# Optimization experiments

Measured on AMD Instinct MI355X. Metric: run time of the kernel, lower is better.

The kernel has to match this reference:

```python
import jax, jax.numpy as jnp
import numpy as np
from jax import lax

S = 8192      # total tokens
HID = 1280    # hidden_size
H = 16        # num_heads
D = HID // H  # head_dim = 80
NSEG = 8      # number of equal-length segments (images)


def rotate_half(x):
    half = x.shape[-1] // 2
    return jnp.concatenate([-x[..., half:], x[..., :half]], axis=-1)


def setup_inputs() -> dict:
    key = jax.random.key(0)
    k1, k2, k3, k4 = jax.random.split(key, 4)
    hidden_states = jax.random.normal(k1, (S, HID), dtype=jnp.float32)
    # rotary embeddings: angles repeated over both halves, as in standard vision RoPE
    theta = jax.random.uniform(k2, (S, D // 2), dtype=jnp.float32) * (2.0 * np.pi)
    freqs = jnp.concatenate([theta, theta], axis=-1)  # [S, D]
    cos = jnp.cos(freqs)
    sin = jnp.sin(freqs)
    qkv_kernel = jax.random.normal(k3, (HID, 3, H, D), dtype=jnp.float32) * 0.02
    qkv_bias = jnp.zeros((3, H, D), dtype=jnp.float32)
    proj_kernel = jax.random.normal(k4, (H * D, HID), dtype=jnp.float32) * 0.02
    proj_bias = jnp.zeros((HID,), dtype=jnp.float32)
    cu_seqlens = jnp.arange(NSEG + 1, dtype=jnp.int32) * (S // NSEG)
    return {
        "hidden_states": hidden_states, "cos": cos, "sin": sin,
        "qkv_kernel": qkv_kernel, "qkv_bias": qkv_bias,
        "proj_kernel": proj_kernel, "proj_bias": proj_bias,
        "cu_seqlens": cu_seqlens,
    }


def reference(hidden_states, cos, sin, qkv_kernel, qkv_bias, proj_kernel, proj_bias, cu_seqlens):
    P = lax.Precision.HIGHEST
    seq, dtype = hidden_states.shape[0], hidden_states.dtype
    # fused QKV projection: [S, 3, H, D]
    qkv = jnp.einsum('sd,dtnh->stnh', hidden_states, qkv_kernel, precision=P) + qkv_bias
    q, k, v = qkv[:, 0], qkv[:, 1], qkv[:, 2]
    # rotary position embedding in fp32 (as in original)
    cf = cos[:, None, :].astype(jnp.float32)
    sf = sin[:, None, :].astype(jnp.float32)
    qf = q.astype(jnp.float32)
    kf = k.astype(jnp.float32)
    q = (qf * cf + rotate_half(qf) * sf).astype(dtype)
    k = (kf * cf + rotate_half(kf) * sf).astype(dtype)
    # block-diagonal attention over equal-length segments from cu_seqlens
    n_seg = cu_seqlens.shape[0] - 1
    L = seq // n_seg  # segment length (uniform segments)
    head_dim = q.shape[-1]
    scale = head_dim ** (-0.5)
    qs = q.reshape(n_seg, L, H, head_dim)
    ks = k.reshape(n_seg, L, H, head_dim)
    vs = v.reshape(n_seg, L, H, head_dim)
    logits = jnp.einsum('bqhd,bkhd->bhqk', qs, ks, precision=P) * scale
    attn = jax.nn.softmax(logits.astype(jnp.float32), axis=-1).astype(dtype)
    out = jnp.einsum('bhqk,bkhd->bqhd', attn, vs, precision=P).reshape(seq, H * head_dim)
    return jnp.einsum('se,ed->sd', out, proj_kernel, precision=P) + proj_bias
```

## Files before the change

kernel.cpp:

```cpp
#include <hip/hip_runtime.h>

#define S_LEN 8192
#define HID   1280
#define NHEAD 16
#define HD    80
#define NQKV  3840
#define VTS   8256

#define GLOBAL_AS __attribute__((address_space(1)))
#define LDS_AS    __attribute__((address_space(3)))

typedef __attribute__((ext_vector_type(8))) short bf16x8;
typedef __attribute__((ext_vector_type(4))) float f32x4;
typedef __attribute__((ext_vector_type(4))) unsigned short u16x4;
typedef __attribute__((ext_vector_type(8))) unsigned short u16x8;
typedef __attribute__((ext_vector_type(2))) unsigned int u32x2;

__device__ __forceinline__ unsigned short f2bf(float f) {
    union { float f; unsigned int u; } v; v.f = f;
    unsigned int r = v.u + 0x7FFFu + ((v.u >> 16) & 1u);
    return (unsigned short)(r >> 16);
}
__device__ __forceinline__ float bf2f(unsigned short h) {
    union { unsigned int u; float f; } v; v.u = ((unsigned int)h) << 16;
    return v.f;
}
__device__ __forceinline__ unsigned int cvt_pk_bf16(float a, float b) {
    unsigned int r;
    asm("v_cvt_pk_bf16_f32 %0, %1, %2" : "=v"(r) : "v"(a), "v"(b));
    return r;
}

__global__ __launch_bounds__(256) void k_cvt(const float* __restrict__ src,
                                             unsigned short* __restrict__ dst,
                                             unsigned short* __restrict__ vbz, int n4)
{
    int i = blockIdx.x * 256 + threadIdx.x;
    if (blockIdx.x == 0 && threadIdx.x < 4)
        ((u16x8*)vbz)[threadIdx.x] = (u16x8)(unsigned short)0;
    if (i >= n4) return;
    f32x4 v = *(const f32x4*)&src[(size_t)i * 4];
    u16x4 o;
    o[0] = f2bf(v[0]); o[1] = f2bf(v[1]); o[2] = f2bf(v[2]); o[3] = f2bf(v[3]);
    *(u16x4*)&dst[(size_t)i * 4] = o;
}

__global__ __launch_bounds__(256) void k_wt(const float* __restrict__ W,
                                            unsigned short* __restrict__ Wt,
                                            int R, int C)
{
    __shared__ float T[32][33];
    int r0 = blockIdx.y * 32, c0 = blockIdx.x * 32;
    int tr = threadIdx.x >> 3, tc = (threadIdx.x & 7) * 4;
    f32x4 v = *(const f32x4*)&W[(size_t)(r0 + tr) * C + c0 + tc];
    T[tr][tc + 0] = v[0]; T[tr][tc + 1] = v[1];
    T[tr][tc + 2] = v[2]; T[tr][tc + 3] = v[3];
    __syncthreads();
    int c = threadIdx.x >> 3, r4 = (threadIdx.x & 7) * 4;
    u16x4 o;
    o[0] = f2bf(T[r4 + 0][c]); o[1] = f2bf(T[r4 + 1][c]);
    o[2] = f2bf(T[r4 + 2][c]); o[3] = f2bf(T[r4 + 3][c]);
    *(u16x4*)&Wt[(size_t)(c0 + c) * R + r0 + r4] = o;
}

__global__ __launch_bounds__(512, 2) void k_qkv256(
    const unsigned short* __restrict__ A,
    const unsigned short* __restrict__ Bt,
    const float* __restrict__ bias,
    unsigned short* __restrict__ q0, unsigned short* __restrict__ k0p,
    unsigned short* __restrict__ vt)
{
    __shared__ __align__(16) unsigned short As[2][2][16][64][8];
    __shared__ __align__(16) unsigned short Bs[2][2][16][64][8];
    const int tid = threadIdx.x;
    const int w = tid >> 6, l = tid & 63;
    const int qg = l & 15, g = l >> 4;
    const int wm = w >> 2, wn = w & 3;
    const int wm8 = wm * 8, wn4 = wn * 4;

    const int bid = blockIdx.x;
    const int xcd = bid & 7, t = bid >> 3;
    const int bm0 = (xcd * 4 + (t & 3)) * 256;
    const int bn0 = (t >> 2) * 256;

    const unsigned short* ga = A + (size_t)(bm0 + w * 16 + qg) * HID + g * 8;
    const unsigned short* gb = Bt + (size_t)(bn0 + w * 16 + qg) * HID + g * 8;

#define SG_A(d, ks, kcol) do {                                                  \
    __builtin_amdgcn_global_load_lds((const GLOBAL_AS unsigned int*)(ga + (kcol)), \
        (LDS_AS unsigned int*)&As[d][ks][w][0][0], 16, 0, 0);                   \
    __builtin_amdgcn_global_load_lds((const GLOBAL_AS unsigned int*)(ga + (size_t)128 * HID + (kcol)), \
        (LDS_AS unsigned int*)&As[d][ks][8 + w][0][0], 16, 0, 0); } while (0)
#define SG_B(d, ks, kcol) do {                                                  \
    __builtin_amdgcn_global_load_lds((const GLOBAL_AS unsigned int*)(gb + (kcol)), \
        (LDS_AS unsigned int*)&Bs[d][ks][w][0][0], 16, 0, 0);                   \
    __builtin_amdgcn_global_load_lds((const GLOBAL_AS unsigned int*)(gb + (size_t)128 * HID + (kcol)), \
        (LDS_AS unsigned int*)&Bs[d][ks][8 + w][0][0], 16, 0, 0); } while (0)

#define RD_A4(d, ks, fb) do {                                                   \
    af[0] = *(const bf16x8*)&As[d][ks][wm8 + (fb) + 0][l][0];                   \
    af[1] = *(const bf16x8*)&As[d][ks][wm8 + (fb) + 1][l][0];                   \
    af[2] = *(const bf16x8*)&As[d][ks][wm8 + (fb) + 2][l][0];                   \
    af[3] = *(const bf16x8*)&As[d][ks][wm8 + (fb) + 3][l][0]; } while (0)
#define RD_B4(d, ks) do {                                                       \
    bf[0] = *(const bf16x8*)&Bs[d][ks][wn4 + 0][l][0];                          \
    bf[1] = *(const bf16x8*)&Bs[d][ks][wn4 + 1][l][0];                          \
    bf[2] = *(const bf16x8*)&Bs[d][ks][wn4 + 2][l][0];                          \
    bf[3] = *(const bf16x8*)&Bs[d][ks][wn4 + 3][l][0]; } while (0)

#define MFMAQ(base) do {                                                        \
    _Pragma("unroll")                                                           \
    for (int m = 0; m < 4; ++m)                                                 \
        _Pragma("unroll")                                                       \
        for (int n = 0; n < 4; ++n)                                             \
            acc[(base) + m][n] = __builtin_amdgcn_mfma_f32_16x16x32_bf16(       \
                af[m], bf[n], acc[(base) + m][n], 0, 0, 0); } while (0)

#define BARW() do { __builtin_amdgcn_s_barrier();                               \
    asm volatile("s_waitcnt lgkmcnt(0)" ::: "memory");                          \
    __builtin_amdgcn_sched_barrier(0);                                          \
    __builtin_amdgcn_s_setprio(1); } while (0)
#define BARC() do { __builtin_amdgcn_s_setprio(0);                              \
    __builtin_amdgcn_s_barrier();                                               \
    __builtin_amdgcn_sched_barrier(0); } while (0)
#define BARC_VM4() do { __builtin_amdgcn_s_setprio(0);                          \
    asm volatile("s_waitcnt vmcnt(4)" ::: "memory");                            \
    __builtin_amdgcn_s_barrier();                                               \
    __builtin_amdgcn_sched_barrier(0); } while (0)
#define BARC_VM0() do { __builtin_amdgcn_s_setprio(0);                          \
    asm volatile("s_waitcnt vmcnt(0)" ::: "memory");                            \
    __builtin_amdgcn_s_barrier();                                               \
    __builtin_amdgcn_sched_barrier(0); } while (0)

    f32x4 acc[8][4];
#pragma unroll
    for (int m = 0; m < 8; ++m)
#pragma unroll
        for (int n = 0; n < 4; ++n) acc[m][n] = (f32x4){0.f, 0.f, 0.f, 0.f};

    SG_A(0, 0, 0);  SG_B(0, 0, 0);
    SG_A(0, 1, 32); SG_B(0, 1, 32);
    SG_A(1, 0, 64); SG_B(1, 0, 64);
    asm volatile("s_waitcnt vmcnt(4)" ::: "memory");
    __builtin_amdgcn_s_barrier();
    __builtin_amdgcn_sched_barrier(0);

    const int NIT = HID / 128;
    for (int j = 0; j < NIT; ++j) {
        const bool st = (j + 1 < NIT);
        const int c1 = j * 128 + 96;
        const int c2 = j * 128 + 128;
        const int c2b = j * 128 + 160;
        const int c3 = j * 128 + 192;
        bf16x8 af[4], bf[4];

        RD_A4(0, 0, 0); RD_B4(0, 0);
        SG_A(1, 1, c1);
        BARW(); MFMAQ(0); BARC();
        RD_A4(0, 0, 4);
        SG_B(1, 1, c1);
        BARW(); MFMAQ(4); BARC();
        RD_A4(0, 1, 0); RD_B4(0, 1);
        if (st) SG_A(0, 0, c2);
        BARW(); MFMAQ(0); BARC();
        RD_A4(0, 1, 4);
        if (st) SG_B(0, 0, c2);
        BARW(); MFMAQ(4);
        if (st) BARC_VM4(); else BARC_VM0();
        RD_A4(1, 0, 0); RD_B4(1, 0);
        if (st) SG_A(0, 1, c2b);
        BARW(); MFMAQ(0); BARC();
        RD_A4(1, 0, 4);
        if (st) SG_B(0, 1, c2b);
        BARW(); MFMAQ(4); BARC();
        RD_A4(1, 1, 0); RD_B4(1, 1);
        if (st) SG_A(1, 0, c3);
        BARW(); MFMAQ(0); BARC();
        RD_A4(1, 1, 4);
        if (st) SG_B(1, 0, c3);
        BARW(); MFMAQ(4);
        if (st) BARC_VM4(); else BARC_VM0();
    }
#undef SG_A
#undef SG_B
#undef RD_A4
#undef RD_B4
#undef MFMAQ
#undef BARW
#undef BARC
#undef BARC_VM4
#undef BARC_VM0

    const int t3 = bn0 / HID;
    if (t3 < 2) {
        unsigned short* dst = (t3 == 0) ? q0 : k0p;
        const int colbase = bn0 - t3 * HID + wn * 64 + qg;
        float bv[4];
#pragma unroll
        for (int n = 0; n < 4; ++n) bv[n] = bias[bn0 + wn * 64 + n * 16 + qg];
#pragma unroll
        for (int m = 0; m < 8; ++m)
#pragma unroll
            for (int r = 0; r < 4; ++r) {
                const int row = bm0 + wm * 128 + m * 16 + g * 4 + r;
                unsigned short* drow = dst + (size_t)row * HID + colbase;
#pragma unroll
                for (int n = 0; n < 4; ++n)
                    drow[n * 16] = f2bf(acc[m][n][r] + bv[n]);
            }
    } else {
        const int colbase = bn0 - 2 * HID + wn * 64;
#pragma unroll
        for (int n = 0; n < 4; ++n) {
            const int vcol = colbase + n * 16 + qg;
            const float bv = bias[bn0 + wn * 64 + n * 16 + qg];
            unsigned short* dcol = vt + (size_t)vcol * VTS + bm0 + wm * 128 + g * 4;
#pragma unroll
            for (int m = 0; m < 8; ++m) {
                u16x4 o;
#pragma unroll
                for (int r = 0; r < 4; ++r) o[r] = f2bf(acc[m][n][r] + bv);
                *(u16x4*)&dcol[m * 16] = o;
            }
        }
    }
}

__global__ __launch_bounds__(256) void k_rope(
    unsigned short* __restrict__ qb, unsigned short* __restrict__ kb,
    const float* __restrict__ cosb, const float* __restrict__ sinb)
{
    const float SCQ = 0.11180339887498949f * 1.44269504088896340f;
    int idx = blockIdx.x * 256 + threadIdx.x;
    if (idx >= S_LEN * NHEAD * 10) return;
    int s = idx / 160;
    int rem = idx - s * 160;
    int nh = rem / 10, h4 = (rem - nh * 10) * 4;
    size_t base = (size_t)s * HID + nh * HD + h4;
    f32x4 c0 = *(const f32x4*)&cosb[s * HD + h4];
    f32x4 c1 = *(const f32x4*)&cosb[s * HD + h4 + 40];
    f32x4 s0 = *(const f32x4*)&sinb[s * HD + h4];
    f32x4 s1 = *(const f32x4*)&sinb[s * HD + h4 + 40];
    u16x4 qa = *(const u16x4*)&qb[base];
    u16x4 qb4 = *(const u16x4*)&qb[base + 40];
    u16x4 ka = *(const u16x4*)&kb[base];
    u16x4 kb4 = *(const u16x4*)&kb[base + 40];
    u16x4 o0, o1, p0, p1;
#pragma unroll
    for (int j = 0; j < 4; ++j) {
        float qaf = bf2f(qa[j]), qbf = bf2f(qb4[j]);
        o0[j] = f2bf((qaf * c0[j] - qbf * s0[j]) * SCQ);
        o1[j] = f2bf((qbf * c1[j] + qaf * s1[j]) * SCQ);
        float kaf = bf2f(ka[j]), kbf = bf2f(kb4[j]);
        p0[j] = f2bf(kaf * c0[j] - kbf * s0[j]);
        p1[j] = f2bf(kbf * c1[j] + kaf * s1[j]);
    }
    *(u16x4*)&qb[base] = o0;
    *(u16x4*)&qb[base + 40] = o1;
    *(u16x4*)&kb[base] = p0;
    *(u16x4*)&kb[base + 40] = p1;
}

__global__ __launch_bounds__(256) void k_attn(
    const unsigned short* __restrict__ qb, const unsigned short* __restrict__ kbuf,
    const unsigned short* __restrict__ vt, unsigned short* __restrict__ ao)
{
    __shared__ __align__(16) unsigned short Ks[2][64][104];
    __shared__ __align__(16) unsigned short Vs[2][80][64];
    __shared__ __align__(16) unsigned short Pls[4][2][16][68];

    const int tid = threadIdx.x;
    const int w = tid >> 6, l = tid & 63;
    const int qg = l & 15, g = l >> 4;
    const int wb = w << 6;
    const int vxor = (qg & 7) << 4;

    const int b = blockIdx.x;
    const int xcd = b & 7, j = b >> 3;
    const int p = xcd * 16 + (j >> 3);
    const int qt = j & 7;
    const int seg = p >> 4, head = p & 15;
    const int row0 = seg * 1024 + qt * 128 + w * 32;
    const size_t hoff = (size_t)head * HD;
    const int vhead = head * HD;
    const int kb0 = seg * 1024;

#define STAGE(bi, kr0_)                                                        \
    {                                                                          \
        const int kr0s = (kr0_);                                               \
        _Pragma("unroll")                                                      \
        for (int i = 0; i < 4; ++i) {                                          \
            const int u = i * 256 + tid;                                       \
            if (u < 832) {                                                     \
                const int r = u / 13, cu = (u - r * 13) * 8;                   \
                __builtin_amdgcn_global_load_lds(                              \
                    (const GLOBAL_AS unsigned int*)&kbuf[(size_t)(kr0s + r) * HID + hoff + cu], \
                    (LDS_AS unsigned int*)((LDS_AS unsigned short*)&Ks[bi][0][0] + (size_t)(i * 256 + wb) * 8), \
                    16, 0, 0);                                                 \
            }                                                                  \
        }                                                                      \
        _Pragma("unroll")                                                      \
        for (int i = 0; i < 3; ++i) {                                          \
            const int u = i * 256 + tid;                                       \
            if (u < 640) {                                                     \
                const int r = u >> 3;                                          \
                const int cs = ((u & 7) * 16) ^ ((r & 7) << 4);                \
                __builtin_amdgcn_global_load_lds(                              \
                    (const GLOBAL_AS unsigned int*)&vt[(size_t)(vhead + r) * VTS + kr0s + (cs >> 1)], \
                    (LDS_AS unsigned int*)((LDS_AS unsigned short*)&Vs[bi][0][0] + (size_t)(i * 256 + wb) * 8), \
                    16, 0, 0);                                                 \
            }                                                                  \
        }                                                                      \
    }

#define COMPUTE(bi)                                                            \
    {                                                                          \
        f32x4 st[2][4];                                                        \
        _Pragma("unroll")                                                      \
        for (int s = 0; s < 2; ++s)                                            \
            _Pragma("unroll")                                                  \
            for (int kn = 0; kn < 4; ++kn) st[s][kn] = (f32x4){0.f, 0.f, 0.f, 0.f}; \
        __builtin_amdgcn_s_setprio(1);                                         \
        _Pragma("unroll")                                                      \
        for (int ks = 0; ks < 3; ++ks)                                         \
            _Pragma("unroll")                                                  \
            for (int kn = 0; kn < 4; ++kn) {                                   \
                bf16x8 kf = *(const bf16x8*)&Ks[bi][kn * 16 + qg][ks * 32 + g * 8]; \
                st[0][kn] = __builtin_amdgcn_mfma_f32_16x16x32_bf16(kf, qf[0][ks], st[0][kn], 0, 0, 0); \
                st[1][kn] = __builtin_amdgcn_mfma_f32_16x16x32_bf16(kf, qf[1][ks], st[1][kn], 0, 0, 0); \
            }                                                                  \
        __builtin_amdgcn_s_setprio(0);                                         \
        _Pragma("unroll")                                                      \
        for (int s = 0; s < 2; ++s) {                                          \
            float psum = 0.f;                                                  \
            _Pragma("unroll")                                                  \
            for (int kn = 0; kn < 4; ++kn) {                                   \
                float p0 = exp2f(st[s][kn][0]);                                \
                float p1 = exp2f(st[s][kn][1]);                                \
                float p2 = exp2f(st[s][kn][2]);                                \
                float p3 = exp2f(st[s][kn][3]);                                \
                psum += (p0 + p1) + (p2 + p3);                                 \
                u32x2 pk;                                                      \
                pk[0] = cvt_pk_bf16(p0, p1);                                   \
                pk[1] = cvt_pk_bf16(p2, p3);                                   \
                *(u32x2*)&Pls[w][s][qg][kn * 16 + g * 4] = pk;                 \
            }                                                                  \
            psum += __shfl_xor(psum, 16, 64);                                  \
            psum += __shfl_xor(psum, 32, 64);                                  \
            lsum[s] += psum;                                                   \
        }                                                                      \
        __builtin_amdgcn_s_setprio(1);                                         \
        _Pragma("unroll")                                                      \
        for (int ks = 0; ks < 2; ++ks) {                                       \
            bf16x8 pf0 = *(const bf16x8*)&Pls[w][0][qg][ks * 32 + g * 8];      \
            bf16x8 pf1 = *(const bf16x8*)&Pls[w][1][qg][ks * 32 + g * 8];      \
            _Pragma("unroll")                                                  \
            for (int d = 0; d < 5; ++d) {                                      \
                bf16x8 vf = *(const bf16x8*)((const unsigned short*)&Vs[bi][0][0] + \
                    (d * 16 + qg) * 64 + (((ks * 64 + g * 16) ^ vxor) >> 1));  \
                acc[0][d] = __builtin_amdgcn_mfma_f32_16x16x32_bf16(vf, pf0, acc[0][d], 0, 0, 0); \
                acc[1][d] = __builtin_amdgcn_mfma_f32_16x16x32_bf16(vf, pf1, acc[1][d], 0, 0, 0); \
            }                                                                  \
        }                                                                      \
        __builtin_amdgcn_s_setprio(0);                                         \
    }

    bf16x8 qf[2][3];
#pragma unroll
    for (int s = 0; s < 2; ++s)
#pragma unroll
        for (int ks = 0; ks < 3; ++ks) {
            if (ks < 2 || g < 2)
                qf[s][ks] = *(const bf16x8*)&qb[(size_t)(row0 + s * 16 + qg) * HID + hoff + ks * 32 + g * 8];
            else
                qf[s][ks] = (bf16x8)(short)0;
        }

    float lsum[2] = {0.f, 0.f};
    f32x4 acc[2][5];
#pragma unroll
    for (int s = 0; s < 2; ++s)
#pragma unroll
        for (int d = 0; d < 5; ++d) acc[s][d] = (f32x4){0.f, 0.f, 0.f, 0.f};

    STAGE(0, kb0);
    __syncthreads();
    for (int ch = 0; ch < 16; ch += 2) {
        if (ch + 1 < 16) STAGE(1, kb0 + (ch + 1) * 64);
        COMPUTE(0);
        __syncthreads();
        if (ch + 2 < 16) STAGE(0, kb0 + (ch + 2) * 64);
        COMPUTE(1);
        __syncthreads();
    }

#pragma unroll
    for (int s = 0; s < 2; ++s) {
        const float inv = 1.0f / lsum[s];
        const int orow = row0 + s * 16 + qg;
#pragma unroll
        for (int d = 0; d < 5; ++d) {
            u16x4 o;
#pragma unroll
            for (int r = 0; r < 4; ++r) o[r] = f2bf(acc[s][d][r] * inv);
            *(u16x4*)&ao[(size_t)orow * HID + hoff + d * 16 + g * 4] = o;
        }
    }
#undef STAGE
#undef COMPUTE
}

__global__ __launch_bounds__(256) void k_proj(
    const unsigned short* __restrict__ A,
    const unsigned short* __restrict__ Bt,
    const float* __restrict__ bias, float* __restrict__ out)
{
    __shared__ __align__(16) unsigned short As[128][32];
    __shared__ __align__(16) unsigned short Bs[128][32];
    const int tid = threadIdx.x;
    const int w = tid >> 6, l = tid & 63;
    const int qg = l & 15, g = l >> 4;
    const int wr = w >> 1, wc = w & 1;
    const int bid = blockIdx.x;
    const int xcd = bid & 7, t = bid >> 3;
    const int bm0 = (xcd * 8 + (t & 7)) * 128;
    const int bn0 = (t >> 3) * 128;

    f32x4 acc[4][4];
#pragma unroll
    for (int m = 0; m < 4; ++m)
#pragma unroll
        for (int n = 0; n < 4; ++n) acc[m][n] = (f32x4){0.f, 0.f, 0.f, 0.f};

    const int lr = l >> 2, lc = (l & 3) * 8;
    const unsigned short* ga = A + (size_t)(bm0 + w * 16 + lr) * HID + lc;
    const unsigned short* gb = Bt + (size_t)(bn0 + w * 16 + lr) * HID + lc;
    LDS_AS unsigned int* la0 = (LDS_AS unsigned int*)&As[w * 16][0];
    LDS_AS unsigned int* la1 = (LDS_AS unsigned int*)&As[w * 16 + 64][0];
    LDS_AS unsigned int* lb0 = (LDS_AS unsigned int*)&Bs[w * 16][0];
    LDS_AS unsigned int* lb1 = (LDS_AS unsigned int*)&Bs[w * 16 + 64][0];

    for (int k0 = 0; k0 < HID; k0 += 32) {
        __syncthreads();
        __builtin_amdgcn_global_load_lds((const GLOBAL_AS unsigned int*)(ga + k0), la0, 16, 0, 0);
        __builtin_amdgcn_global_load_lds((const GLOBAL_AS unsigned int*)(ga + (size_t)64 * HID + k0), la1, 16, 0, 0);
        __builtin_amdgcn_global_load_lds((const GLOBAL_AS unsigned int*)(gb + k0), lb0, 16, 0, 0);
        __builtin_amdgcn_global_load_lds((const GLOBAL_AS unsigned int*)(gb + (size_t)64 * HID + k0), lb1, 16, 0, 0);
        __syncthreads();
        bf16x8 af[4], bff[4];
#pragma unroll
        for (int m = 0; m < 4; ++m) af[m] = *(const bf16x8*)&As[wr * 64 + m * 16 + qg][g * 8];
#pragma unroll
        for (int n = 0; n < 4; ++n) bff[n] = *(const bf16x8*)&Bs[wc * 64 + n * 16 + qg][g * 8];
#pragma unroll
        for (int m = 0; m < 4; ++m)
#pragma unroll
            for (int n = 0; n < 4; ++n)
                acc[m][n] = __builtin_amdgcn_mfma_f32_16x16x32_bf16(af[m], bff[n], acc[m][n], 0, 0, 0);
    }

#pragma unroll
    for (int n = 0; n < 4; ++n) {
        const int col = bn0 + wc * 64 + n * 16 + qg;
        const float bv = bias[col];
#pragma unroll
        for (int m = 0; m < 4; ++m)
#pragma unroll
            for (int r = 0; r < 4; ++r) {
                const int row = bm0 + wr * 64 + m * 16 + g * 4 + r;
                out[(size_t)row * HID + col] = acc[m][n][r] + bv;
            }
    }
}

extern "C" void kernel_launch(void* const* d_in, const int* in_sizes, int n_in,
                              void* d_out, int out_size, void* d_ws, size_t ws_size,
                              hipStream_t stream)
{
    (void)in_sizes; (void)n_in; (void)out_size; (void)ws_size;
    const float* hidden = (const float*)d_in[0];
    const float* cosb   = (const float*)d_in[1];
    const float* sinb   = (const float*)d_in[2];
    const float* qkv_w  = (const float*)d_in[3];
    const float* qkv_b  = (const float*)d_in[4];
    const float* proj_w = (const float*)d_in[5];
    const float* proj_b = (const float*)d_in[6];

    float* out = (float*)d_out;
    unsigned short* ws = (unsigned short*)d_ws;
    const size_t n = (size_t)S_LEN * HID;
    unsigned short* hb     = ws;
    unsigned short* wqkvt  = hb + n;
    unsigned short* wprojt = wqkvt + (size_t)NQKV * HID;
    unsigned short* qb     = wprojt + (size_t)HID * HID;
    unsigned short* kb     = qb + n;
    unsigned short* vb     = kb + n;
    unsigned short* vt     = vb + n;
    unsigned short* aob    = vt + (size_t)NHEAD * HD * VTS;

    k_cvt<<<(int)((n / 4 + 255) / 256), 256, 0, stream>>>(hidden, hb, vb, (int)(n / 4));
    dim3 gw1(NQKV / 32, HID / 32);
    k_wt<<<gw1, 256, 0, stream>>>(qkv_w, wqkvt, HID, NQKV);
    dim3 gw2(HID / 32, HID / 32);
    k_wt<<<gw2, 256, 0, stream>>>(proj_w, wprojt, HID, HID);

    k_qkv256<<<480, 512, 0, stream>>>(hb, wqkvt, qkv_b, qb, kb, vt);

    k_rope<<<(S_LEN * NHEAD * 10 + 255) / 256, 256, 0, stream>>>(qb, kb, cosb, sinb);

    k_attn<<<1024, 256, 0, stream>>>(qb, kb, vt, aob);

    k_proj<<<640, 256, 0, stream>>>(aob, wprojt, proj_b, out);
}
```

Baseline: 255.3 us.

## Transpose softmax probabilities in registers via cross-lane shuffles instead of LDS

Removes the per-wave LDS staging buffer for the bf16 probability tile. The C-layout of the QK^T MFMA output is now rearranged into the B-operand layout for the PV MFMA with selects and two rounds of __shfl_xor, so no LDS writes or reads are needed. Dropping that buffer also cuts shared memory per block, and launch bounds now request 3 blocks per CU to raise occupancy. The cost is extra VALU/DPP shuffle work and register pressure, and the occupancy hint may force spills.

Measured after the change: 257.3 us. About the same (+0.8%).

```diff
diff --git a/kernel.cpp b/kernel.cpp
--- a/kernel.cpp
+++ b/kernel.cpp
@@ -15,6 +15,7 @@
 typedef __attribute__((ext_vector_type(4))) unsigned short u16x4;
 typedef __attribute__((ext_vector_type(8))) unsigned short u16x8;
 typedef __attribute__((ext_vector_type(2))) unsigned int u32x2;
+typedef __attribute__((ext_vector_type(4))) unsigned int u32x4;
 
 __device__ __forceinline__ unsigned short f2bf(float f) {
     union { float f; unsigned int u; } v; v.f = f;
@@ -261,19 +262,21 @@
     *(u16x4*)&kb[base + 40] = p1;
 }
 
-__global__ __launch_bounds__(256) void k_attn(
+__global__ __launch_bounds__(256, 3) void k_attn(
     const unsigned short* __restrict__ qb, const unsigned short* __restrict__ kbuf,
     const unsigned short* __restrict__ vt, unsigned short* __restrict__ ao)
 {
     __shared__ __align__(16) unsigned short Ks[2][64][104];
     __shared__ __align__(16) unsigned short Vs[2][80][64];
-    __shared__ __align__(16) unsigned short Pls[4][2][16][68];
 
     const int tid = threadIdx.x;
     const int w = tid >> 6, l = tid & 63;
     const int qg = l & 15, g = l >> 4;
     const int wb = w << 6;
     const int vxor = (qg & 7) << 4;
+    const bool bb = (g & 2) != 0;
+    const bool cb = ((g ^ (g >> 1)) & 1) != 0;
+    const bool og = (g & 1) != 0;
 
     const int b = blockIdx.x;
     const int xcd = b & 7, j = b >> 3;
@@ -330,9 +333,11 @@
                 st[1][kn] = __builtin_amdgcn_mfma_f32_16x16x32_bf16(kf, qf[1][ks], st[1][kn], 0, 0, 0); \
             }                                                                  \
         __builtin_amdgcn_s_setprio(0);                                         \
+        bf16x8 pfr[2][2];                                                      \
         _Pragma("unroll")                                                      \
         for (int s = 0; s < 2; ++s) {                                          \
             float psum = 0.f;                                                  \
+            unsigned int E[4][2];                                              \
             _Pragma("unroll")                                                  \
             for (int kn = 0; kn < 4; ++kn) {                                   \
                 float p0 = exp2f(st[s][kn][0]);                                \
@@ -340,20 +345,49 @@
                 float p2 = exp2f(st[s][kn][2]);                                \
                 float p3 = exp2f(st[s][kn][3]);                                \
                 psum += (p0 + p1) + (p2 + p3);                                 \
-                u32x2 pk;                                                      \
-                pk[0] = cvt_pk_bf16(p0, p1);                                   \
-                pk[1] = cvt_pk_bf16(p2, p3);                                   \
-                *(u32x2*)&Pls[w][s][qg][kn * 16 + g * 4] = pk;                 \
+                E[kn][0] = cvt_pk_bf16(p0, p1);                                \
+                E[kn][1] = cvt_pk_bf16(p2, p3);                                \
             }                                                                  \
             psum += __shfl_xor(psum, 16, 64);                                  \
             psum += __shfl_xor(psum, 32, 64);                                  \
             lsum[s] += psum;                                                   \
+            const unsigned int oc0x = bb ? E[1][0] : E[0][0];                  \
+            const unsigned int oc0y = bb ? E[1][1] : E[0][1];                  \
+            const unsigned int oc1x = bb ? E[3][0] : E[2][0];                  \
+            const unsigned int oc1y = bb ? E[3][1] : E[2][1];                  \
+            const unsigned int sa0x = bb ? E[0][0] : E[1][0];                  \
+            const unsigned int sa0y = bb ? E[0][1] : E[1][1];                  \
+            const unsigned int sa1x = bb ? E[2][0] : E[3][0];                  \
+            const unsigned int sa1y = bb ? E[2][1] : E[3][1];                  \
+            const unsigned int rx0x = __shfl_xor(sa0x, 32, 64);                \
+            const unsigned int rx0y = __shfl_xor(sa0y, 32, 64);                \
+            const unsigned int rx1x = __shfl_xor(sa1x, 32, 64);                \
+            const unsigned int rx1y = __shfl_xor(sa1y, 32, 64);                \
+            const unsigned int kp0x = cb ? rx0x : oc0x;                        \
+            const unsigned int kp0y = cb ? rx0y : oc0y;                        \
+            const unsigned int kp1x = cb ? rx1x : oc1x;                        \
+            const unsigned int kp1y = cb ? rx1y : oc1y;                        \
+            const unsigned int sb0x = cb ? oc0x : rx0x;                        \
+            const unsigned int sb0y = cb ? oc0y : rx0y;                        \
+            const unsigned int sb1x = cb ? oc1x : rx1x;                        \
+            const unsigned int sb1y = cb ? oc1y : rx1y;                        \
+            const unsigned int rb0x = __shfl_xor(sb0x, 16, 64);                \
+            const unsigned int rb0y = __shfl_xor(sb0y, 16, 64);                \
+            const unsigned int rb1x = __shfl_xor(sb1x, 16, 64);                \
+            const unsigned int rb1y = __shfl_xor(sb1y, 16, 64);                \
+            u32x4 t0, t1;                                                      \
+            t0[0] = og ? rb0x : kp0x; t0[1] = og ? rb0y : kp0y;                \
+            t0[2] = og ? kp0x : rb0x; t0[3] = og ? kp0y : rb0y;                \
+            t1[0] = og ? rb1x : kp1x; t1[1] = og ? rb1y : kp1y;                \
+            t1[2] = og ? kp1x : rb1x; t1[3] = og ? kp1y : rb1y;                \
+            pfr[s][0] = __builtin_bit_cast(bf16x8, t0);                        \
+            pfr[s][1] = __builtin_bit_cast(bf16x8, t1);                        \
         }                                                                      \
         __builtin_amdgcn_s_setprio(1);                                         \
         _Pragma("unroll")                                                      \
         for (int ks = 0; ks < 2; ++ks) {                                       \
-            bf16x8 pf0 = *(const bf16x8*)&Pls[w][0][qg][ks * 32 + g * 8];      \
-            bf16x8 pf1 = *(const bf16x8*)&Pls[w][1][qg][ks * 32 + g * 8];      \
+            bf16x8 pf0 = pfr[0][ks];                                           \
+            bf16x8 pf1 = pfr[1][ks];                                           \
             _Pragma("unroll")                                                  \
             for (int d = 0; d < 5; ++d) {                                      \
                 bf16x8 vf = *(const bf16x8*)((const unsigned short*)&Vs[bi][0][0] + \
```
